# Kernel optimization log

Hardware: AMD Instinct MI355X
Metric: run time of the kernel (lower is better)

Reference implementation:

```python
import jax, jax.numpy as jnp
import numpy as np

N = 2048
NONGT = 2048
EMB = 64
GROUP = 16
FEAT = 256
DM = 1024  # dim[0] == dim[1]
DHEAD = DM // GROUP  # 64


def setup_inputs() -> dict:
    key = jax.random.key(0)
    ks = jax.random.split(key, 12)
    s = lambda fan_in: 1.0 / np.sqrt(fan_in)
    return {
        "roi_feat": jax.random.normal(ks[0], (N, FEAT), jnp.float32),
        "position_embedding": jax.random.uniform(ks[1], (N, NONGT, EMB), jnp.float32),
        "fc1_w": jax.random.normal(ks[2], (GROUP, EMB), jnp.float32) * s(EMB),
        "fc1_b": jnp.zeros((GROUP,), jnp.float32),
        "fc2_w": jax.random.normal(ks[3], (DM, FEAT), jnp.float32) * s(FEAT),
        "fc2_b": jnp.zeros((DM,), jnp.float32),
        "fc3_w": jax.random.normal(ks[4], (DM, FEAT), jnp.float32) * s(FEAT),
        "fc3_b": jnp.zeros((DM,), jnp.float32),
        "conv_w": jax.random.normal(ks[5], (FEAT, GROUP * FEAT), jnp.float32) * s(GROUP * FEAT),
        "conv_b": jnp.zeros((FEAT,), jnp.float32),
        "nongt_dim": NONGT,
    }


def reference(roi_feat, position_embedding, fc1_w, fc1_b, fc2_w, fc2_b,
              fc3_w, fc3_b, conv_w, conv_b, nongt_dim):
    nongt_roi_feat = roi_feat[:nongt_dim, :]                      # [M, FEAT]
    # position bias: relu(fc1(pe)) -> [N, M, G] -> [N, G, M]
    pos1 = jax.nn.relu(jnp.einsum('nme,ge->nmg', position_embedding, fc1_w) + fc1_b)
    aff_weight = jnp.transpose(pos1, (0, 2, 1))                   # [N, G, M]
    # grouped Q, K
    q = roi_feat @ fc2_w.T + fc2_b                                # [N, DM]
    q = q.reshape(-1, GROUP, DHEAD)                               # [N, G, d]
    k = nongt_roi_feat @ fc3_w.T + fc3_b                          # [M, DM]
    k = k.reshape(-1, GROUP, DHEAD)                               # [M, G, d]
    scale = 1.0 / np.sqrt(float(DHEAD))
    aff = jnp.einsum('ngd,mgd->ngm', q, k) * scale                # [N, G, M]
    weighted = jnp.log(jnp.maximum(aff_weight, 1e-6)) + aff
    aff_softmax = jax.nn.softmax(weighted, axis=-1)               # [N, G, M]
    out_t = jnp.einsum('ngm,mc->ngc', aff_softmax, nongt_roi_feat)  # [N, G, FEAT]
    flat = out_t.reshape(out_t.shape[0], GROUP * FEAT)            # channel order g*FEAT + c
    return flat @ conv_w.T + conv_b                               # [N, FEAT]
```

## Files before the change

kernel.cpp:

```cpp
#include <hip/hip_runtime.h>
#include <hip/hip_bf16.h>

#define NQ   2048
#define NK   2048
#define EMB  64
#define GRP  16
#define FEAT 256

typedef __bf16 bf16x8 __attribute__((ext_vector_type(8)));
typedef __bf16 bf16x4 __attribute__((ext_vector_type(4)));
typedef float  f32x4  __attribute__((ext_vector_type(4)));

#define MFMA(a, b, c) __builtin_amdgcn_mfma_f32_16x16x32_bf16((a), (b), (c), 0, 0, 0)

typedef __attribute__((address_space(3))) unsigned int  lds_u32;
typedef __attribute__((address_space(1))) unsigned int  glb_u32;

static __device__ __forceinline__ bf16x8 cvt8(float4 a, float4 b) {
    bf16x8 r;
    r[0] = (__bf16)a.x; r[1] = (__bf16)a.y; r[2] = (__bf16)a.z; r[3] = (__bf16)a.w;
    r[4] = (__bf16)b.x; r[5] = (__bf16)b.y; r[6] = (__bf16)b.z; r[7] = (__bf16)b.w;
    return r;
}

__global__ void prep_roiT(const float* __restrict__ roi, __bf16* __restrict__ roiT) {
    __shared__ float tile[64][65];
    const int tid = threadIdx.x;
    const int m0 = (blockIdx.x >> 2) * 64, c0 = (blockIdx.x & 3) * 64;
    const int tr = tid >> 4, tc = tid & 15;
#pragma unroll
    for (int ch = 0; ch < 4; ++ch) {
        int r = ch * 16 + tr;
        float4 v = *(const float4*)(roi + (m0 + r) * 256 + c0 + tc * 4);
        tile[r][tc * 4 + 0] = v.x; tile[r][tc * 4 + 1] = v.y;
        tile[r][tc * 4 + 2] = v.z; tile[r][tc * 4 + 3] = v.w;
    }
    __syncthreads();
#pragma unroll
    for (int ch = 0; ch < 4; ++ch) {
        int crow = ch * 16 + tr;
        int mm = tc * 4;
        bf16x4 o;
        o[0] = (__bf16)tile[mm + 0][crow]; o[1] = (__bf16)tile[mm + 1][crow];
        o[2] = (__bf16)tile[mm + 2][crow]; o[3] = (__bf16)tile[mm + 3][crow];
        *(bf16x4*)(roiT + (c0 + crow) * 2048 + m0 + mm) = o;
    }
}

__global__ void prep_cast(const float* __restrict__ in, __bf16* __restrict__ out, int n4) {
    int idx = blockIdx.x * blockDim.x + threadIdx.x;
    for (int i = idx; i < n4; i += gridDim.x * blockDim.x) {
        float4 v = ((const float4*)in)[i];
        bf16x4 o;
        o[0] = (__bf16)v.x; o[1] = (__bf16)v.y; o[2] = (__bf16)v.z; o[3] = (__bf16)v.w;
        ((bf16x4*)out)[i] = o;
    }
}

__global__ void prep_qk(const float* __restrict__ roi,
                        const float* __restrict__ Wq, const float* __restrict__ bq,
                        const float* __restrict__ Wk, const float* __restrict__ bk,
                        __bf16* __restrict__ outq, __bf16* __restrict__ outk) {
    const float* W    = blockIdx.y ? Wk   : Wq;
    const float* bias = blockIdx.y ? bk   : bq;
    __bf16*      out  = blockIdx.y ? outk : outq;
    const int tid = threadIdx.x, l = tid & 63, wid = tid >> 6;
    const int n0 = (blockIdx.x >> 2) * 16;
    const int dmB = (blockIdx.x & 3) * 256 + wid * 64;
    const int lr = l & 15, lk = l >> 4;
    f32x4 acc[4];
#pragma unroll
    for (int i = 0; i < 4; ++i) acc[i] = (f32x4){0.f, 0.f, 0.f, 0.f};
    for (int k0 = 0; k0 < 256; k0 += 32) {
        const float* ap = roi + (n0 + lr) * 256 + k0 + lk * 8;
        bf16x8 af = cvt8(*(const float4*)ap, *(const float4*)(ap + 4));
#pragma unroll
        for (int cf = 0; cf < 4; ++cf) {
            const float* bp = W + (dmB + cf * 16 + lr) * 256 + k0 + lk * 8;
            acc[cf] = MFMA(af, cvt8(*(const float4*)bp, *(const float4*)(bp + 4)), acc[cf]);
        }
    }
#pragma unroll
    for (int cf = 0; cf < 4; ++cf) {
        int dm = dmB + cf * 16 + lr;
        float bv = bias[dm];
        int g = dm >> 6, d = dm & 63;
#pragma unroll
        for (int ri = 0; ri < 4; ++ri) {
            int n = n0 + lk * 4 + ri;
            out[(g * 2048 + n) * 64 + d] = (__bf16)(acc[cf][ri] + bv);
        }
    }
}

__launch_bounds__(256, 4)
__global__ void w_gemm(const float* __restrict__ pe,
                       const float* __restrict__ fc1w,
                       const float* __restrict__ fc1b,
                       __bf16* __restrict__ wg) {
    const int tid = threadIdx.x, l = tid & 63, wid = tid >> 6;
    const int lr = l & 15, lk = l >> 4;
    const long n = blockIdx.x >> 2;
    const int mbase = (blockIdx.x & 3) * 512 + wid * 128;

    bf16x8 fcB[2];
#pragma unroll
    for (int s = 0; s < 2; ++s) {
        const float* p = fc1w + lr * 64 + s * 32 + lk * 8;
        fcB[s] = cvt8(*(const float4*)p, *(const float4*)(p + 4));
    }
    const float bias = fc1b[lr];

    const float* pebase = pe + (n * 2048 + mbase + lr) * 64 + lk * 8;
    __bf16* obase = wg + (n * 16 + lr) * 2048 + mbase + lk * 4;

#pragma unroll 4
    for (int it = 0; it < 8; ++it) {
        const float* p0 = pebase + it * 16 * 64;
        f32x4 c = (f32x4){0.f, 0.f, 0.f, 0.f};
        c = MFMA(cvt8(*(const float4*)(p0),      *(const float4*)(p0 + 4)),  fcB[0], c);
        c = MFMA(cvt8(*(const float4*)(p0 + 32), *(const float4*)(p0 + 36)), fcB[1], c);
        bf16x4 o;
#pragma unroll
        for (int ri = 0; ri < 4; ++ri)
            o[ri] = (__bf16)fmaxf(fmaxf(c[ri] + bias, 0.f), 1e-6f);
        *(bf16x4*)(obase + it * 16) = o;
    }
}

#define P_BASE 32768
__launch_bounds__(256, 2)
__global__ void relation_attn(const __bf16* __restrict__ wg,
                              const __bf16* __restrict__ qb,
                              const __bf16* __restrict__ kb,
                              const __bf16* __restrict__ roiT,
                              __bf16* __restrict__ flat) {
    __shared__ __align__(16) unsigned char smem[40960];
    const int tid = threadIdx.x;
    const int l   = tid & 63;
    const int wid = tid >> 6;
    const int n0  = (blockIdx.x >> 1) * 8;
    const int ghalf = blockIdx.x & 1;
    const int lr  = l & 15;
    const int lk  = l >> 4;
    const int gh  = lk >> 1;
    const int nqh = lk & 1;
    const int g2  = ghalf * 8 + wid * 2;
    const int gA  = g2 + gh;

    bf16x8 qa[2][2];
#pragma unroll
    for (int gi = 0; gi < 2; ++gi)
#pragma unroll
        for (int s = 0; s < 2; ++s)
            qa[gi][s] = *(const bf16x8*)(qb + (long)((g2 + gi) * 2048 + n0 + (lr & 7)) * 64 + s * 32 + lk * 8);

    f32x4 acc[16];
#pragma unroll
    for (int i = 0; i < 16; ++i) acc[i] = (f32x4){0.f, 0.f, 0.f, 0.f};
    float dsum[4] = {0.f, 0.f, 0.f, 0.f};

    const __bf16* wptr = wg + (long)((n0 + (nqh << 2)) * 16 + gA) * 2048 + lr;

    for (int t = 0; t < 32; ++t) {
        const int m0t = t * 64;
        __syncthreads();

        {
            const int crow = l >> 3, slot = l & 7;
#pragma unroll
            for (int i = 0; i < 8; ++i) {
                int c = wid * 64 + i * 8 + crow;
                int D = slot ^ (c & 7);
                const __bf16* gp = roiT + c * 2048 + m0t + D * 8;
                __builtin_amdgcn_global_load_lds(
                    (const glb_u32*)(const void*)gp,
                    (lds_u32*)(void*)(smem + wid * 8192 + i * 1024), 16, 0, 0);
            }
        }

        float wlv[4][4];
#pragma unroll
        for (int mf = 0; mf < 4; ++mf)
#pragma unroll
            for (int ri = 0; ri < 4; ++ri)
                wlv[mf][ri] = (float)wptr[(long)ri * 32768 + m0t + mf * 16];

        f32x4 a0[4], a1[4];
#pragma unroll
        for (int mf = 0; mf < 4; ++mf) {
            const __bf16* kp = kb + (long)(g2 * 2048 + m0t + mf * 16 + lr) * 64 + lk * 8;
            bf16x8 k0 = *(const bf16x8*)(kp);
            bf16x8 k1 = *(const bf16x8*)(kp + 32);
            f32x4 z = (f32x4){0.f, 0.f, 0.f, 0.f};
            z = MFMA(qa[0][0], k0, z);
            z = MFMA(qa[0][1], k1, z);
            a0[mf] = z;
        }
#pragma unroll
        for (int mf = 0; mf < 4; ++mf) {
            const __bf16* kp = kb + (long)((g2 + 1) * 2048 + m0t + mf * 16 + lr) * 64 + lk * 8;
            bf16x8 k0 = *(const bf16x8*)(kp);
            bf16x8 k1 = *(const bf16x8*)(kp + 32);
            f32x4 z = (f32x4){0.f, 0.f, 0.f, 0.f};
            z = MFMA(qa[1][0], k0, z);
            z = MFMA(qa[1][1], k1, z);
            a1[mf] = z;
        }

#pragma unroll
        for (int mf = 0; mf < 4; ++mf) {
            int mm = mf * 16 + lr;
#pragma unroll
            for (int ri = 0; ri < 4; ++ri) {
                float a = gh ? a1[mf][ri] : a0[mf][ri];
                int n2 = (nqh << 2) + ri;
                float pv = wlv[mf][ri] * __expf(a * 0.125f);
                dsum[ri] += pv;
                int rp = ((gA & 7) << 3) + n2;
                int poff = (rp << 7) + ((mm ^ (n2 << 3)) << 1);
                *(__bf16*)(smem + P_BASE + poff) = (__bf16)pv;
            }
        }

        __syncthreads();

        {
            const int rpA = wid * 16 + lr;
            const int QA = (rpA & 7) << 3;
#pragma unroll
            for (int s = 0; s < 2; ++s) {
                bf16x8 pA = *(const bf16x8*)(smem + P_BASE + (rpA << 7)
                                             + (((s * 32 + lk * 8) ^ QA) << 1));
#pragma unroll
                for (int cf = 0; cf < 16; ++cf) {
                    int c = cf * 16 + lr;
                    bf16x8 rB = *(const bf16x8*)(smem + c * 128
                                                 + (((s * 4 + lk) ^ (c & 7)) << 4));
                    acc[cf] = MFMA(pA, rB, acc[cf]);
                }
            }
        }
    }

    float inv[4];
#pragma unroll
    for (int ri = 0; ri < 4; ++ri) {
        float v = dsum[ri];
        v += __shfl_xor(v, 1); v += __shfl_xor(v, 2);
        v += __shfl_xor(v, 4); v += __shfl_xor(v, 8);
        inv[ri] = 1.0f / v;
    }
#pragma unroll
    for (int cf = 0; cf < 16; ++cf) {
        int c = cf * 16 + lr;
#pragma unroll
        for (int ri = 0; ri < 4; ++ri) {
            int n2 = (nqh << 2) + ri;
            flat[(long)(n0 + n2) * 4096 + gA * 256 + c] = (__bf16)(acc[cf][ri] * inv[ri]);
        }
    }
}

__launch_bounds__(256)
__global__ void conv_gemm(const __bf16* __restrict__ flat, const __bf16* __restrict__ cw,
                          const float* __restrict__ cb, float* __restrict__ out) {
    const int tid = threadIdx.x, l = tid & 63, wid = tid >> 6;
    const int n0 = (blockIdx.x >> 1) * 16;
    const int j0 = (blockIdx.x & 1) * 128 + wid * 32;
    const int lr = l & 15, lk = l >> 4;
    f32x4 acc[2] = {(f32x4){0.f, 0.f, 0.f, 0.f}, (f32x4){0.f, 0.f, 0.f, 0.f}};
#pragma unroll 4
    for (int k0 = 0; k0 < 4096; k0 += 32) {
        bf16x8 af = *(const bf16x8*)(flat + (long)(n0 + lr) * 4096 + k0 + lk * 8);
#pragma unroll
        for (int cf = 0; cf < 2; ++cf) {
            bf16x8 bfr = *(const bf16x8*)(cw + (long)(j0 + cf * 16 + lr) * 4096 + k0 + lk * 8);
            acc[cf] = MFMA(af, bfr, acc[cf]);
        }
    }
#pragma unroll
    for (int cf = 0; cf < 2; ++cf) {
        int j = j0 + cf * 16 + lr;
        float bv = cb[j];
#pragma unroll
        for (int ri = 0; ri < 4; ++ri)
            out[(n0 + lk * 4 + ri) * 256 + j] = acc[cf][ri] + bv;
    }
}

extern "C" void kernel_launch(void* const* d_in, const int* in_sizes, int n_in,
                              void* d_out, int out_size, void* d_ws, size_t ws_size,
                              hipStream_t stream) {
    const float* roi  = (const float*)d_in[0];
    const float* pe   = (const float*)d_in[1];
    const float* fc1w = (const float*)d_in[2];
    const float* fc1b = (const float*)d_in[3];
    const float* fc2w = (const float*)d_in[4];
    const float* fc2b = (const float*)d_in[5];
    const float* fc3w = (const float*)d_in[6];
    const float* fc3b = (const float*)d_in[7];
    const float* cw   = (const float*)d_in[8];
    const float* cb   = (const float*)d_in[9];
    float* out = (float*)d_out;

    unsigned char* ws = (unsigned char*)d_ws;
    __bf16* roiT   = (__bf16*)(ws);
    __bf16* convwb = (__bf16*)(ws + (1ull  << 20));
    __bf16* qb     = (__bf16*)(ws + (3ull  << 20));
    __bf16* kb     = (__bf16*)(ws + (7ull  << 20));
    __bf16* flat   = (__bf16*)(ws + (11ull << 20));
    __bf16* wg     = (__bf16*)(ws + (27ull << 20));

    w_gemm<<<8192, 256, 0, stream>>>(pe, fc1w, fc1b, wg);
    prep_roiT<<<128, 256, 0, stream>>>(roi, roiT);
    prep_cast<<<512, 256, 0, stream>>>(cw, convwb, (256 * 4096) / 4);
    prep_qk<<<dim3(512, 2), 256, 0, stream>>>(roi, fc2w, fc2b, fc3w, fc3b, qb, kb);
    relation_attn<<<512, 256, 0, stream>>>(wg, qb, kb, roiT, flat);
    conv_gemm<<<256, 256, 0, stream>>>(flat, convwb, cb, out);
}
```

Before: 499.2 us.

## Stage position-bias weights through LDS with async prefetch of next tile

Replaces per-thread scattered bf16 global loads of the position-bias weights with coalesced 16-byte global_load_lds copies into a swizzled LDS buffer. The next tile's weights are prefetched after the mid-iteration barrier so the copy overlaps the PV matmul phase. This adds 8 KB of LDS per block and relies on barriers to order the async writes against reads of the single buffer.

```diff
diff --git a/kernel.cpp b/kernel.cpp
--- a/kernel.cpp
+++ b/kernel.cpp
@@ -128,14 +128,15 @@
     }
 }
 
-#define P_BASE 32768
+#define P_BASE  32768
+#define WG_BASE 40960
 __launch_bounds__(256, 2)
 __global__ void relation_attn(const __bf16* __restrict__ wg,
                               const __bf16* __restrict__ qb,
                               const __bf16* __restrict__ kb,
                               const __bf16* __restrict__ roiT,
                               __bf16* __restrict__ flat) {
-    __shared__ __align__(16) unsigned char smem[40960];
+    __shared__ __align__(16) unsigned char smem[49152];
     const int tid = threadIdx.x;
     const int l   = tid & 63;
     const int wid = tid >> 6;
@@ -160,7 +161,18 @@
     for (int i = 0; i < 16; ++i) acc[i] = (f32x4){0.f, 0.f, 0.f, 0.f};
     float dsum[4] = {0.f, 0.f, 0.f, 0.f};
 
-    const __bf16* wptr = wg + (long)((n0 + (nqh << 2)) * 16 + gA) * 2048 + lr;
+#pragma unroll
+    for (int i = 0; i < 2; ++i) {
+        int ch   = wid * 128 + i * 64 + l;
+        int row  = ch >> 3;
+        int n2s  = row & 7;
+        int glos = row >> 3;
+        int slot = (ch & 7) ^ n2s;
+        const __bf16* gp = wg + ((long)(n0 + n2s) * 16 + ghalf * 8 + glos) * 2048 + slot * 8;
+        __builtin_amdgcn_global_load_lds(
+            (const glb_u32*)(const void*)gp,
+            (lds_u32*)(void*)(smem + WG_BASE + ch * 16), 16, 0, 0);
+    }
 
     for (int t = 0; t < 32; ++t) {
         const int m0t = t * 64;
@@ -179,13 +191,6 @@
             }
         }
 
-        float wlv[4][4];
-#pragma unroll
-        for (int mf = 0; mf < 4; ++mf)
-#pragma unroll
-            for (int ri = 0; ri < 4; ++ri)
-                wlv[mf][ri] = (float)wptr[(long)ri * 32768 + m0t + mf * 16];
-
         f32x4 a0[4], a1[4];
 #pragma unroll
         for (int mf = 0; mf < 4; ++mf) {
@@ -215,7 +220,11 @@
             for (int ri = 0; ri < 4; ++ri) {
                 float a = gh ? a1[mf][ri] : a0[mf][ri];
                 int n2 = (nqh << 2) + ri;
-                float pv = wlv[mf][ri] * __expf(a * 0.125f);
+                int rowA = ((gA & 7) << 3) + n2;
+                int chunkA = (((mf << 1) + (lr >> 3)) ^ n2);
+                float wv = (float)*(const __bf16*)(smem + WG_BASE + (rowA << 7)
+                                                   + (chunkA << 4) + ((lr & 7) << 1));
+                float pv = wv * __expf(a * 0.125f);
                 dsum[ri] += pv;
                 int rp = ((gA & 7) << 3) + n2;
                 int poff = (rp << 7) + ((mm ^ (n2 << 3)) << 1);
@@ -224,6 +233,23 @@
         }
 
         __syncthreads();
+
+        if (t < 31) {
+            const int m0n = m0t + 64;
+#pragma unroll
+            for (int i = 0; i < 2; ++i) {
+                int ch   = wid * 128 + i * 64 + l;
+                int row  = ch >> 3;
+                int n2s  = row & 7;
+                int glos = row >> 3;
+                int slot = (ch & 7) ^ n2s;
+                const __bf16* gp = wg + ((long)(n0 + n2s) * 16 + ghalf * 8 + glos) * 2048
+                                      + m0n + slot * 8;
+                __builtin_amdgcn_global_load_lds(
+                    (const glb_u32*)(const void*)gp,
+                    (lds_u32*)(void*)(smem + WG_BASE + ch * 16), 16, 0, 0);
+            }
+        }
 
         {
             const int rpA = wid * 16 + lr;
```

Measured after the change: 501.1 us. About the same (+0.4%).
